# Performance work log

Hardware: AMD Instinct MI355X
Metric: run time of the kernel (lower is better)

The kernel has to match this reference:

```python
import jax, jax.numpy as jnp
import numpy as np
import math

B, L, D = 8, 2048, 768
ORDER, EMB = 128, 5
FFT = 2 * L
MIN_DECAY = math.log(0.01) / 1.5   # slow_decay_pct = 1.5
MAX_DECAY = math.log(0.01) / 0.3   # fast_decay_pct = 0.3
SHIFT = 0.0


def _pos_emb(seq_len, emb_dim):
    # pos_emb_init from the source: [t, Re(z), Im(z)] with bands = (emb_dim-1)//2
    bands = (emb_dim - 1) // 2
    t = jnp.linspace(0.0, 1.0, seq_len)[None, :, None]
    t_res = jnp.linspace(0.0, seq_len - 1, seq_len)[None, :, None]
    w = 2.0 * jnp.pi * t_res / seq_len
    f = jnp.linspace(1e-4, bands - 1, bands)[None, None]
    zc = jnp.exp(-1j * f * w)
    return jnp.concatenate([t, zc.real, zc.imag], axis=-1).astype(jnp.float32)  # (1, L, EMB)


def setup_inputs() -> dict:
    key = jax.random.key(0)
    ks = jax.random.split(key, 16)
    s = 0.02
    return {
        "u": jax.random.normal(ks[0], (B, L, D), jnp.float32),
        "in_W": jax.random.normal(ks[1], (D, 3 * D), jnp.float32) * s,
        "in_b": jnp.zeros((3 * D,), jnp.float32),
        "out_W": jax.random.normal(ks[2], (D, D), jnp.float32) * s,
        "out_b": jnp.zeros((D,), jnp.float32),
        "x1_s": jax.random.normal(ks[3], (D, 4), jnp.float32) * 0.25,
        "x2_s": jax.random.normal(ks[4], (D, 4), jnp.float32) * 0.25,
        "v_s": jax.random.normal(ks[5], (D, 4), jnp.float32) * 0.25,
        "x1_sb": jax.random.normal(ks[6], (D,), jnp.float32) * 0.1,
        "x2_sb": jax.random.normal(ks[7], (D,), jnp.float32) * 0.1,
        "v_sb": jax.random.normal(ks[8], (D,), jnp.float32) * 0.1,
        "D_bias": jax.random.normal(ks[9], (D,), jnp.float32),
        "z": _pos_emb(L, EMB),
        "sin_freq": 10.0 * jnp.ones((1, ORDER), jnp.float32),   # hyena_w = 10
        "eo_mat": jax.random.normal(ks[10], (1, EMB, ORDER), jnp.float32) * 0.3,
        "eo_bias": jnp.zeros((1, ORDER), jnp.float32),
        "oo1_mat": jax.random.normal(ks[11], (1, ORDER, ORDER), jnp.float32) * 0.08,
        "oo1_bias": jnp.zeros((1, ORDER), jnp.float32),
        "oo2_mat": jax.random.normal(ks[12], (1, ORDER, ORDER), jnp.float32) * 0.08,
        "oo2_bias": jnp.zeros((1, ORDER), jnp.float32),
        "oh_mat": jax.random.normal(ks[13], (1, ORDER, D), jnp.float32) * 0.08,
    }


def _depthwise4(x, w, b):
    # torch Conv1d(groups=3D, kernel=4, padding=3) truncated to [:L] == causal conv, left pad 3
    out = jax.lax.conv_general_dilated(
        x, w[:, None, :], window_strides=(1,), padding=[(3, 0)],
        dimension_numbers=("NCH", "OIH", "NCH"), feature_group_count=x.shape[1])
    return out + b[None, :, None]


def _hyena_filter(z, sin_freq, eo_mat, eo_bias, oo1_mat, oo1_bias, oo2_mat, oo2_bias, oh_mat):
    # then exponential decay modulation (exp_mod_in_place_fwd), channels=1, reverse=0.
    f = sin_freq[:, None, :]                                       # (1, 1, ORDER)
    h = jnp.sin(f * (jnp.einsum("cle,ceo->clo", z, eo_mat) + eo_bias[:, None, :]))
    h = jnp.sin(f * (jnp.einsum("clo,cop->clp", h, oo1_mat) + oo1_bias[:, None, :]))
    h = jnp.sin(f * (jnp.einsum("clo,cop->clp", h, oo2_mat) + oo2_bias[:, None, :]))
    k = jnp.einsum("clo,coh->clh", h, oh_mat)                      # (1, L, D)
    t = jnp.linspace(0.0, 1.0, k.shape[1])
    deltas = jnp.abs(jnp.linspace(MIN_DECAY, MAX_DECAY, k.shape[2]))
    k = k * (jnp.exp(-t[None, :, None] * deltas[None, None, :]) + SHIFT)
    return k[0].T                                                  # (D, L)


def _forward(u, in_W, in_b, out_W, out_b, x1_s, x2_s, v_s, x1_sb, x2_sb, v_sb,
             D_bias, z, sin_freq, eo_mat, eo_bias, oo1_mat, oo1_bias,
             oo2_mat, oo2_bias, oh_mat):
    seqlen = u.shape[1]
    k = _hyena_filter(z, sin_freq, eo_mat, eo_bias, oo1_mat, oo1_bias, oo2_mat, oo2_bias, oh_mat)
    x1x2v = u @ in_W + in_b                                        # (B, L, 3D)
    x1, x2, v = jnp.split(x1x2v, 3, axis=-1)
    x1 = jnp.transpose(x1, (0, 2, 1))                              # (B, D, L)
    x2 = jnp.transpose(x2, (0, 2, 1))
    v = jnp.transpose(v, (0, 2, 1))
    x1 = _depthwise4(x1, x1_s, x1_sb)
    x2 = _depthwise4(x2, x2_s, x2_sb)
    v = _depthwise4(v, v_s, v_sb)
    v = v * x1                                                     # first gate
    k_f = jnp.fft.rfft(k.astype(jnp.float32), n=FFT)               # (D, FFT//2+1)
    v_f = jnp.fft.rfft(v.astype(jnp.float32), n=FFT)               # (B, D, FFT//2+1)
    y = jnp.fft.irfft(v_f * k_f[None], n=FFT)[..., :seqlen]        # long FFT conv
    y = y + v * D_bias[None, :, None]                              # skip term
    y = y * x2                                                     # second gate
    y = jnp.transpose(y, (0, 2, 1))                                # (B, L, D)
    return y @ out_W + out_b


def reference(u, in_W, in_b, out_W, out_b, x1_s, x2_s, v_s, x1_sb, x2_sb, v_sb,
              D_bias, z, sin_freq, eo_mat, eo_bias, oo1_mat, oo1_bias,
              oo2_mat, oo2_bias, oh_mat):
    return _forward(u, in_W, in_b, out_W, out_b, x1_s, x2_s, v_s, x1_sb, x2_sb, v_sb,
                    D_bias, z, sin_freq, eo_mat, eo_bias, oo1_mat, oo1_bias,
                    oo2_mat, oo2_bias, oh_mat)
```

## Files before the change

kernel.cpp:

```cpp
#include <hip/hip_runtime.h>


typedef __bf16 bf16x8 __attribute__((ext_vector_type(8)));
typedef float  f32x4  __attribute__((ext_vector_type(4)));

#define AS1 __attribute__((address_space(1)))
#define AS3 __attribute__((address_space(3)))
#define GLD16(gp, lp) __builtin_amdgcn_global_load_lds((AS1 void*)(void*)(gp), (AS3 void*)(void*)(lp), 16, 0, 0)

#define LGKM_BAR       __asm__ __volatile__("s_waitcnt lgkmcnt(0)\n\ts_barrier" ::: "memory")
#define VM_LGKM_BAR(N) __asm__ __volatile__("s_waitcnt vmcnt(" #N ") lgkmcnt(0)\n\ts_barrier" ::: "memory")

__device__ __forceinline__ unsigned short f2b(float f) {
    unsigned u = __builtin_bit_cast(unsigned, f);
    unsigned r = (u + 0x7fffu + ((u >> 16) & 1u)) >> 16;
    return (unsigned short)r;
}
__device__ __forceinline__ float b2f(unsigned short h) {
    unsigned u = ((unsigned)h) << 16;
    return __builtin_bit_cast(float, u);
}
__device__ __forceinline__ float b2f_lo(unsigned u) {
    return __builtin_bit_cast(float, u << 16);
}
__device__ __forceinline__ float b2f_hi(unsigned u) {
    return __builtin_bit_cast(float, u & 0xffff0000u);
}

__device__ __forceinline__ float2 cmul(float2 a, float2 b) {
    return make_float2(a.x * b.x - a.y * b.y, a.x * b.y + a.y * b.x);
}
__device__ __forceinline__ float2 cadd(float2 a, float2 b) { return make_float2(a.x + b.x, a.y + b.y); }
__device__ __forceinline__ float2 csub(float2 a, float2 b) { return make_float2(a.x - b.x, a.y - b.y); }

#define BFLY(i,j)   { float2 ta=x[i], tb=x[j]; x[i]=cadd(ta,tb); x[j]=csub(ta,tb); }
#define BFLYW(i,j,w){ float2 ta=x[i], tb=x[j]; x[i]=cadd(ta,tb); x[j]=cmul(csub(ta,tb),(w)); }
#define BFLYI(i,j)  { float2 ta=x[i], tb=x[j]; x[i]=cadd(ta,tb); float2 tt=csub(ta,tb); x[j]=make_float2(-dd*tt.y, dd*tt.x); }
#define CSWAP(i,j)  { float2 tt=x[i]; x[i]=x[j]; x[j]=tt; }

template<int DIR, bool UZ>
__device__ __forceinline__ void dft16(float2* x) {
    const float dd = (float)DIR;
    const float C1 = 0.92387953251128674f, S1 = 0.38268343236508977f, R2 = 0.70710678118654752f;
    const float2 W1 = make_float2( C1, dd*S1);
    const float2 W2 = make_float2( R2, dd*R2);
    const float2 W3 = make_float2( S1, dd*C1);
    const float2 W5 = make_float2(-S1, dd*C1);
    const float2 W6 = make_float2(-R2, dd*R2);
    const float2 W7 = make_float2(-C1, dd*S1);
    if (UZ) {
        x[8]  = x[0];
        x[9]  = cmul(x[1], W1);
        x[10] = cmul(x[2], W2);
        x[11] = cmul(x[3], W3);
        x[12] = make_float2(-dd*x[4].y, dd*x[4].x);
        x[13] = cmul(x[5], W5);
        x[14] = cmul(x[6], W6);
        x[15] = cmul(x[7], W7);
    } else {
        BFLY(0,8); BFLYW(1,9,W1); BFLYW(2,10,W2); BFLYW(3,11,W3);
        BFLYI(4,12); BFLYW(5,13,W5); BFLYW(6,14,W6); BFLYW(7,15,W7);
    }
    BFLY(0,4);  BFLYW(1,5,W2);  BFLYI(2,6);   BFLYW(3,7,W6);
    BFLY(8,12); BFLYW(9,13,W2); BFLYI(10,14); BFLYW(11,15,W6);
    BFLY(0,2);  BFLYI(1,3);  BFLY(4,6);   BFLYI(5,7);
    BFLY(8,10); BFLYI(9,11); BFLY(12,14); BFLYI(13,15);
    BFLY(0,1); BFLY(2,3); BFLY(4,5); BFLY(6,7);
    BFLY(8,9); BFLY(10,11); BFLY(12,13); BFLY(14,15);
    CSWAP(1,8); CSWAP(2,4); CSWAP(3,12); CSWAP(5,10); CSWAP(7,14); CSWAP(11,13);
}

__device__ __forceinline__ void twiddle_mul(float2* x, float ang) {
    float s, c; __sincosf(ang, &s, &c);
    float2 w[16];
    w[1] = make_float2(c, s);
    w[2] = cmul(w[1], w[1]);
    w[3] = cmul(w[2], w[1]);  w[4] = cmul(w[2], w[2]);
    w[5] = cmul(w[4], w[1]);  w[6] = cmul(w[4], w[2]);
    w[7] = cmul(w[4], w[3]);  w[8] = cmul(w[4], w[4]);
    w[9]  = cmul(w[8], w[1]); w[10] = cmul(w[8], w[2]);
    w[11] = cmul(w[8], w[3]); w[12] = cmul(w[8], w[4]);
    w[13] = cmul(w[8], w[5]); w[14] = cmul(w[8], w[6]);
    w[15] = cmul(w[8], w[7]);
    #pragma unroll
    for (int k = 1; k < 16; ++k) x[k] = cmul(x[k], w[k]);
}

#define TWO_PI 6.283185307179586f
__device__ __forceinline__ void fft4096_fwd(float2* x, float2* lds, int t) {
    dft16<-1, true>(x);
    twiddle_mul(x, -(float)t * (TWO_PI / 4096.0f));
    #pragma unroll
    for (int k1 = 0; k1 < 16; ++k1) lds[k1 * 272 + t] = x[k1];
    __syncthreads();
    const int hi = t >> 4, lo = t & 15;
    #pragma unroll
    for (int t1 = 0; t1 < 16; ++t1) x[t1] = lds[hi * 272 + t1 * 16 + lo];
    dft16<-1, false>(x);
    twiddle_mul(x, -(float)lo * (TWO_PI / 256.0f));
    __syncthreads();
    #pragma unroll
    for (int k2 = 0; k2 < 16; ++k2) lds[t * 17 + k2] = x[k2];
    __syncthreads();
    #pragma unroll
    for (int t0 = 0; t0 < 16; ++t0) x[t0] = lds[(hi * 16 + t0) * 17 + lo];
    dft16<-1, false>(x);
}

__device__ __forceinline__ void fft4096_inv(float2* x, float2* lds, int t) {
    const int hi = t >> 4, lo = t & 15;
    dft16<1, false>(x);
    __syncthreads();
    #pragma unroll
    for (int t0 = 0; t0 < 16; ++t0) lds[(hi * 16 + t0) * 17 + lo] = x[t0];
    __syncthreads();
    #pragma unroll
    for (int k2 = 0; k2 < 16; ++k2) x[k2] = lds[t * 17 + k2];
    twiddle_mul(x, (float)lo * (TWO_PI / 256.0f));
    dft16<1, false>(x);
    __syncthreads();
    #pragma unroll
    for (int t1 = 0; t1 < 16; ++t1) lds[hi * 272 + t1 * 16 + lo] = x[t1];
    __syncthreads();
    #pragma unroll
    for (int k1 = 0; k1 < 16; ++k1) x[k1] = lds[k1 * 272 + t];
    twiddle_mul(x, (float)t * (TWO_PI / 4096.0f));
    dft16<1, false>(x);
}

__global__ __launch_bounds__(256) void filter_k_kernel(
    const float* __restrict__ z, const float* __restrict__ sf,
    const float* __restrict__ eo, const float* __restrict__ eo_b,
    const float* __restrict__ oo1, const float* __restrict__ oo1_b,
    const float* __restrict__ oo2, const float* __restrict__ oo2_b,
    const float* __restrict__ oh, float* __restrict__ kfil)
{
    __shared__ float h3buf[8][128];
    __shared__ float htmp[2][128];
    const int t = threadIdx.x;
    const int l0 = blockIdx.x * 8;
    const int half = t >> 7;
    const int o = t & 127;
    const float sfo = sf[o];
    for (int p = 0; p < 4; ++p) {
        const int li = p * 2 + half;
        const int l = l0 + li;
        float a = eo_b[o];
        #pragma unroll
        for (int e = 0; e < 5; ++e) a += z[l * 5 + e] * eo[e * 128 + o];
        htmp[half][o] = sinf(sfo * a);
        __syncthreads();
        float a2 = oo1_b[o];
        for (int q = 0; q < 128; ++q) a2 += htmp[half][q] * oo1[q * 128 + o];
        const float h2 = sinf(sfo * a2);
        __syncthreads();
        htmp[half][o] = h2;
        __syncthreads();
        float a3 = oo2_b[o];
        for (int q = 0; q < 128; ++q) a3 += htmp[half][q] * oo2[q * 128 + o];
        h3buf[li][o] = sinf(sfo * a3);
        __syncthreads();
    }
    const float MIND = -3.070113457325394f;
    const float MAXD = -15.350567286626972f;
    for (int c = 0; c < 3; ++c) {
        const int h = t + c * 256;
        float acc[8];
        #pragma unroll
        for (int li = 0; li < 8; ++li) acc[li] = 0.f;
        for (int q = 0; q < 128; ++q) {
            const float w = oh[q * 768 + h];
            #pragma unroll
            for (int li = 0; li < 8; ++li) acc[li] += h3buf[li][q] * w;
        }
        const float delta = fabsf(MIND + (MAXD - MIND) * (float)h * (1.0f / 767.0f));
        #pragma unroll
        for (int li = 0; li < 8; ++li) {
            const int l = l0 + li;
            const float tt = (float)l * (1.0f / 2047.0f);
            kfil[h * 2048 + l] = acc[li] * expf(-tt * delta);
        }
    }
}

__global__ __launch_bounds__(256, 4) void filter_fft_kernel(
    const float* __restrict__ kfil, float2* __restrict__ Kf)
{
    __shared__ float2 lds[4352];
    const int d = blockIdx.x, t = threadIdx.x;
    float2 x[16];
    #pragma unroll
    for (int r = 0; r < 8; ++r) x[r] = make_float2(kfil[d * 2048 + r * 256 + t], 0.f);
    fft4096_fwd(x, lds, t);
    #pragma unroll
    for (int k3 = 0; k3 < 16; ++k3) Kf[d * 4096 + k3 * 256 + t] = x[k3];
}

__global__ __launch_bounds__(256) void convert_u_kernel(
    const float* __restrict__ u, unsigned short* __restrict__ ub)
{
    const int g = blockIdx.x * 256 + threadIdx.x;
    const float4 v = ((const float4*)u)[g];
    uint2 o;
    o.x = (unsigned)f2b(v.x) | ((unsigned)f2b(v.y) << 16);
    o.y = (unsigned)f2b(v.z) | ((unsigned)f2b(v.w) << 16);
    ((uint2*)ub)[g] = o;
}

__global__ __launch_bounds__(256) void transpose_W_kernel(
    const float* __restrict__ W, unsigned short* __restrict__ Wt, int K, int N)
{
    __shared__ float tile[32][33];
    const int n0 = blockIdx.x * 32, k0 = blockIdx.y * 32;
    const int tx = threadIdx.x & 31, ty = threadIdx.x >> 5;
    #pragma unroll
    for (int r = 0; r < 4; ++r) {
        const int kk = ty + r * 8;
        tile[kk][tx] = W[(k0 + kk) * N + n0 + tx];
    }
    __syncthreads();
    #pragma unroll
    for (int r = 0; r < 4; ++r) {
        const int nn = ty + r * 8;
        Wt[(n0 + nn) * K + k0 + tx] = f2b(tile[tx][nn]);
    }
}

__global__ __launch_bounds__(256) void transpose_Y_kernel(
    const unsigned short* __restrict__ Y, unsigned short* __restrict__ Yt)
{
    __shared__ unsigned short tile[32][34];
    const int bx = blockIdx.x;
    const int l0 = (bx & 63) * 32;
    const int tmp = bx >> 6;
    const int d0 = (tmp % 24) * 32;
    const int b  = tmp / 24;
    const int tx = threadIdx.x & 31, ty = threadIdx.x >> 5;
    #pragma unroll
    for (int r = 0; r < 4; ++r) {
        const int dd = ty + r * 8;
        tile[dd][tx] = Y[(b * 768 + d0 + dd) * 2048 + l0 + tx];
    }
    __syncthreads();
    #pragma unroll
    for (int r = 0; r < 4; ++r) {
        const int ll = ty + r * 8;
        Yt[(b * 2048 + l0 + ll) * 768 + d0 + tx] = tile[tx][ll];
    }
}

__global__ __launch_bounds__(512, 2) void gemm256_kernel(
    const unsigned short* __restrict__ A,
    const unsigned short* __restrict__ Bm,
    const float* __restrict__ bias,
    unsigned short* __restrict__ outb,
    float* __restrict__ outf,
    int mode)
{
    extern __shared__ __align__(16) unsigned short lds[];
    unsigned short* As = lds;
    unsigned short* Bs = lds + 32768;
    const int t = threadIdx.x;
    const int wv = t >> 6, lane = t & 63;
    const int row0 = (mode == 0 ? blockIdx.y : blockIdx.x) * 256;
    const int col0 = (mode == 0 ? blockIdx.x : blockIdx.y) * 256;
    const int wr = wv >> 2, wc = wv & 3;
    const int frow = lane & 15, kc = lane >> 4;

    f32x4 acc[8][4] = {};

    const int srow = t >> 3;
    const int cdat = (t & 7) ^ (srow & 7);
    const unsigned short* gA = A  + (row0 + srow) * 768 + cdat * 8;
    const unsigned short* gB = Bm + (col0 + srow) * 768 + cdat * 8;

#define STG_A(buf, q, koff) GLD16(gA + (q) * 49152 + (koff), (char*)As + (buf) * 32768 + (q) * 8192 + wv * 1024)
#define STG_B(buf, q, koff) GLD16(gB + (q) * 49152 + (koff), (char*)Bs + (buf) * 32768 + (q) * 8192 + wv * 1024)

    const int sx = frow & 7;
    const int aRowBase = (wr * 128 + frow) * 64;
    const int bRowBase = (wc * 64 + frow) * 64;
    const int sl0 = ((0 + kc) ^ sx) * 8;
    const int sl1 = ((4 + kc) ^ sx) * 8;

    bf16x8 aF[4][2], bN0[2][2], bN1[2][2];

#define READ_A(buf, mh)                                                         \
    _Pragma("unroll") for (int m = 0; m < 4; ++m) {                             \
        aF[m][0] = *(const bf16x8*)(As + (buf) * 16384 + aRowBase + ((mh) * 4 + m) * 1024 + sl0); \
        aF[m][1] = *(const bf16x8*)(As + (buf) * 16384 + aRowBase + ((mh) * 4 + m) * 1024 + sl1); \
    }
#define READ_B(buf, nh, arr)                                                    \
    _Pragma("unroll") for (int n = 0; n < 2; ++n) {                             \
        arr[n][0] = *(const bf16x8*)(Bs + (buf) * 16384 + bRowBase + ((nh) * 2 + n) * 1024 + sl0); \
        arr[n][1] = *(const bf16x8*)(Bs + (buf) * 16384 + bRowBase + ((nh) * 2 + n) * 1024 + sl1); \
    }
#define MFMA_Q(mh, nh, arr)                                                     \
    __builtin_amdgcn_s_setprio(1);                                              \
    _Pragma("unroll") for (int m = 0; m < 4; ++m)                               \
    _Pragma("unroll") for (int n = 0; n < 2; ++n)                               \
    _Pragma("unroll") for (int ks = 0; ks < 2; ++ks)                            \
        acc[(mh) * 4 + m][(nh) * 2 + n] = __builtin_amdgcn_mfma_f32_16x16x32_bf16( \
            aF[m][ks], arr[n][ks], acc[(mh) * 4 + m][(nh) * 2 + n], 0, 0, 0);   \
    __builtin_amdgcn_s_setprio(0);

    STG_A(0, 0, 0); STG_A(0, 1, 0); STG_A(0, 2, 0); STG_A(0, 3, 0);
    STG_B(0, 0, 0); STG_B(0, 1, 0); STG_B(0, 2, 0); STG_B(0, 3, 0);
    STG_A(1, 0, 64); STG_A(1, 2, 64);
    STG_B(1, 0, 64); STG_B(1, 1, 64); STG_B(1, 2, 64); STG_B(1, 3, 64);
    VM_LGKM_BAR(6);

    for (int i = 0; i < 5; ++i) {
        const int k1 = (2 * i + 1) * 64, k2 = (2 * i + 2) * 64, k3 = (2 * i + 3) * 64;
        READ_A(0, 0); READ_B(0, 0, bN0);
        STG_A(1, 1, k1); STG_A(1, 3, k1);
        MFMA_Q(0, 0, bN0);
        LGKM_BAR;
        READ_B(0, 1, bN1);
        STG_A(0, 0, k2); STG_A(0, 2, k2);
        MFMA_Q(0, 1, bN1);
        LGKM_BAR;
        READ_A(0, 1);
        STG_B(0, 0, k2); STG_B(0, 1, k2);
        MFMA_Q(1, 1, bN1);
        LGKM_BAR;
        STG_B(0, 2, k2); STG_B(0, 3, k2);
        MFMA_Q(1, 0, bN0);
        VM_LGKM_BAR(6);
        READ_A(1, 0); READ_B(1, 0, bN0);
        STG_A(0, 1, k2); STG_A(0, 3, k2);
        MFMA_Q(0, 0, bN0);
        LGKM_BAR;
        READ_B(1, 1, bN1);
        STG_A(1, 0, k3); STG_A(1, 2, k3);
        MFMA_Q(0, 1, bN1);
        LGKM_BAR;
        READ_A(1, 1);
        STG_B(1, 0, k3); STG_B(1, 1, k3);
        MFMA_Q(1, 1, bN1);
        LGKM_BAR;
        STG_B(1, 2, k3); STG_B(1, 3, k3);
        MFMA_Q(1, 0, bN0);
        VM_LGKM_BAR(6);
    }

    {
        READ_A(0, 0); READ_B(0, 0, bN0);
        STG_A(1, 1, 704); STG_A(1, 3, 704);
        MFMA_Q(0, 0, bN0);
        LGKM_BAR;
        READ_B(0, 1, bN1);
        MFMA_Q(0, 1, bN1);
        LGKM_BAR;
        READ_A(0, 1);
        MFMA_Q(1, 1, bN1);
        LGKM_BAR;
        MFMA_Q(1, 0, bN0);
        VM_LGKM_BAR(2);
        READ_A(1, 0); READ_B(1, 0, bN0);
        MFMA_Q(0, 0, bN0);
        LGKM_BAR;
        READ_B(1, 1, bN1);
        MFMA_Q(0, 1, bN1);
        VM_LGKM_BAR(0);
        READ_A(1, 1);
        MFMA_Q(1, 1, bN1);
        MFMA_Q(1, 0, bN0);
    }
#undef READ_A
#undef READ_B
#undef MFMA_Q
#undef STG_A
#undef STG_B

    if (mode == 0) {
        const int part = row0 / 768;
        const int bb = col0 / 2048;
        unsigned short* Xp = outb + (size_t)(part * 8 + bb) * 768 * 2048;
        const int drow0 = row0 - part * 768 + wr * 128 + (lane >> 4) * 4;
        const int lcol0 = col0 - bb * 2048 + wc * 64 + frow;
        #pragma unroll
        for (int m = 0; m < 8; ++m) {
            #pragma unroll
            for (int rr = 0; rr < 4; ++rr) {
                const int dd = drow0 + m * 16 + rr;
                const float bn = bias[row0 + wr * 128 + (lane >> 4) * 4 + m * 16 + rr];
                #pragma unroll
                for (int n = 0; n < 4; ++n)
                    Xp[dd * 2048 + lcol0 + n * 16] = f2b(acc[m][n][rr] + bn);
            }
        }
    } else {
        #pragma unroll
        for (int m = 0; m < 8; ++m) {
            #pragma unroll
            for (int rr = 0; rr < 4; ++rr) {
                const int mm = row0 + wr * 128 + (lane >> 4) * 4 + m * 16 + rr;
                #pragma unroll
                for (int n = 0; n < 4; ++n) {
                    const int nn = col0 + wc * 64 + n * 16 + frow;
                    outf[(size_t)mm * 768 + nn] = acc[m][n][rr] + bias[nn];
                }
            }
        }
    }
}

__device__ __forceinline__ void conv6(const unsigned short* __restrict__ p,
                                      const float* w, float bias, int t, float* out8)
{
    const uint4 m = *(const uint4*)(p + 8 * t);
    uint2 q = make_uint2(0u, 0u);
    if (t) q = *(const uint2*)(p + 8 * t - 4);
    float s[12];
    s[0] = b2f_lo(q.x); s[1] = b2f_hi(q.x); s[2] = b2f_lo(q.y); s[3] = b2f_hi(q.y);
    s[4] = b2f_lo(m.x); s[5] = b2f_hi(m.x); s[6] = b2f_lo(m.y); s[7] = b2f_hi(m.y);
    s[8] = b2f_lo(m.z); s[9] = b2f_hi(m.z); s[10] = b2f_lo(m.w); s[11] = b2f_hi(m.w);
    #pragma unroll
    for (int i = 0; i < 8; ++i)
        out8[i] = bias + w[0] * s[i + 1] + w[1] * s[i + 2] + w[2] * s[i + 3] + w[3] * s[i + 4];
}

__global__ __launch_bounds__(256, 4) void fft_conv_kernel(
    const unsigned short* __restrict__ X, const float2* __restrict__ Kf,
    const float* __restrict__ x1_s, const float* __restrict__ x2_s, const float* __restrict__ v_s,
    const float* __restrict__ x1_sb, const float* __restrict__ x2_sb, const float* __restrict__ v_sb,
    const float* __restrict__ D_bias, unsigned short* __restrict__ Y)
{
    __shared__ __align__(16) float2 lds[4352];
    unsigned* ldsu = (unsigned*)lds;
    const int d = blockIdx.x, jp = blockIdx.y, t = threadIdx.x;
    const int b0 = jp * 2, b1 = b0 + 1;

    float w1[4], w2[4], wv[4];
    #pragma unroll
    for (int j = 0; j < 4; ++j) { w1[j] = x1_s[d * 4 + j]; w2[j] = x2_s[d * 4 + j]; wv[j] = v_s[d * 4 + j]; }
    const float bc1 = x1_sb[d], bc2 = x2_sb[d], bcv = v_sb[d], Db = D_bias[d];

    const unsigned short* px1a = X + ((size_t)(0 * 8 + b0) * 768 + d) * 2048;
    const unsigned short* px2a = X + ((size_t)(1 * 8 + b0) * 768 + d) * 2048;
    const unsigned short* pva  = X + ((size_t)(2 * 8 + b0) * 768 + d) * 2048;
    const unsigned short* px1b = X + ((size_t)(0 * 8 + b1) * 768 + d) * 2048;
    const unsigned short* px2b = X + ((size_t)(1 * 8 + b1) * 768 + d) * 2048;
    const unsigned short* pvb  = X + ((size_t)(2 * 8 + b1) * 768 + d) * 2048;

    {
        float x1a[8], x2a[8], vva[8];
        conv6(px1a, w1, bc1, t, x1a);
        conv6(px2a, w2, bc2, t, x2a);
        conv6(pva,  wv, bcv, t, vva);
        float x1b[8], x2b[8], vvb[8];
        conv6(px1b, w1, bc1, t, x1b);
        conv6(px2b, w2, bc2, t, x2b);
        conv6(pvb,  wv, bcv, t, vvb);
        unsigned vh_pk[8], c2_pk[8];
        #pragma unroll
        for (int i = 0; i < 8; ++i) {
            vh_pk[i] = (unsigned)f2b(vva[i] * x1a[i]) | ((unsigned)f2b(vvb[i] * x1b[i]) << 16);
            c2_pk[i] = (unsigned)f2b(x2a[i]) | ((unsigned)f2b(x2b[i]) << 16);
        }
        *(uint4*)(ldsu + 8 * t)        = make_uint4(vh_pk[0], vh_pk[1], vh_pk[2], vh_pk[3]);
        *(uint4*)(ldsu + 8 * t + 4)    = make_uint4(vh_pk[4], vh_pk[5], vh_pk[6], vh_pk[7]);
        *(uint4*)(ldsu + 2048 + 8 * t)     = make_uint4(c2_pk[0], c2_pk[1], c2_pk[2], c2_pk[3]);
        *(uint4*)(ldsu + 2048 + 8 * t + 4) = make_uint4(c2_pk[4], c2_pk[5], c2_pk[6], c2_pk[7]);
    }
    __syncthreads();

    unsigned vhp[8], c2p[8];
    float2 x[16];
    #pragma unroll
    for (int r = 0; r < 8; ++r) {
        const unsigned u = ldsu[r * 256 + t];
        vhp[r] = u;
        x[r] = make_float2(b2f_lo(u), b2f_hi(u));
    }
    #pragma unroll
    for (int r = 0; r < 8; ++r) c2p[r] = ldsu[2048 + r * 256 + t];

    const float2* kf = Kf + (size_t)d * 4096;
    float2 kfr[16];
    #pragma unroll
    for (int k3 = 0; k3 < 16; ++k3) kfr[k3] = kf[k3 * 256 + t];

    __syncthreads();

    fft4096_fwd(x, lds, t);
    #pragma unroll
    for (int k3 = 0; k3 < 16; ++k3) x[k3] = cmul(x[k3], kfr[k3]);
    fft4096_inv(x, lds, t);

    const float invN = 1.0f / 4096.0f;
    unsigned short* ya = Y + ((size_t)b0 * 768 + d) * 2048;
    unsigned short* yb = Y + ((size_t)b1 * 768 + d) * 2048;
    #pragma unroll
    for (int n1 = 0; n1 < 8; ++n1) {
        const int l = n1 * 256 + t;
        const float va = b2f_lo(vhp[n1]);
        const float vb = b2f_hi(vhp[n1]);
        const float ca = b2f_lo(c2p[n1]);
        const float cb = b2f_hi(c2p[n1]);
        ya[l] = f2b((x[n1].x * invN + va * Db) * ca);
        yb[l] = f2b((x[n1].y * invN + vb * Db) * cb);
    }
}

extern "C" void kernel_launch(void* const* d_in, const int* in_sizes, int n_in,
                              void* d_out, int out_size, void* d_ws, size_t ws_size,
                              hipStream_t stream)
{
    (void)in_sizes; (void)n_in; (void)out_size; (void)ws_size;
    const float* u      = (const float*)d_in[0];
    const float* in_W   = (const float*)d_in[1];
    const float* in_b   = (const float*)d_in[2];
    const float* out_W  = (const float*)d_in[3];
    const float* out_b  = (const float*)d_in[4];
    const float* x1_s   = (const float*)d_in[5];
    const float* x2_s   = (const float*)d_in[6];
    const float* v_s    = (const float*)d_in[7];
    const float* x1_sb  = (const float*)d_in[8];
    const float* x2_sb  = (const float*)d_in[9];
    const float* v_sb   = (const float*)d_in[10];
    const float* D_bias = (const float*)d_in[11];
    const float* z      = (const float*)d_in[12];
    const float* sf     = (const float*)d_in[13];
    const float* eo     = (const float*)d_in[14];
    const float* eo_b   = (const float*)d_in[15];
    const float* oo1    = (const float*)d_in[16];
    const float* oo1_b  = (const float*)d_in[17];
    const float* oo2    = (const float*)d_in[18];
    const float* oo2_b  = (const float*)d_in[19];
    const float* oh     = (const float*)d_in[20];
    float* out = (float*)d_out;

    char* ws = (char*)d_ws;
    unsigned short* Xbf  = (unsigned short*)(ws + 0);
    unsigned short* Ybf  = (unsigned short*)(ws + 75497472);
    unsigned short* ubYt = (unsigned short*)(ws + 100663296);
    unsigned short* Wt   = (unsigned short*)(ws + 125829120);
    unsigned short* W2t  = (unsigned short*)(ws + 129368064);
    float*          kfil = (float*)(ws + 130547712);
    float2*         Kf   = (float2*)(ws + 136839168);

    static int attr_set = 0;
    if (!attr_set) {
        (void)hipFuncSetAttribute(reinterpret_cast<const void*>(gemm256_kernel),
                                  hipFuncAttributeMaxDynamicSharedMemorySize, 131072);
        attr_set = 1;
    }

    filter_k_kernel<<<256, 256, 0, stream>>>(z, sf, eo, eo_b, oo1, oo1_b, oo2, oo2_b, oh, kfil);
    filter_fft_kernel<<<768, 256, 0, stream>>>(kfil, Kf);
    convert_u_kernel<<<12288, 256, 0, stream>>>(u, ubYt);
    transpose_W_kernel<<<dim3(72, 24), 256, 0, stream>>>(in_W, Wt, 768, 2304);
    transpose_W_kernel<<<dim3(24, 24), 256, 0, stream>>>(out_W, W2t, 768, 768);
    gemm256_kernel<<<dim3(64, 9), 512, 131072, stream>>>(Wt, ubYt, in_b, Xbf, nullptr, 0);
    fft_conv_kernel<<<dim3(768, 4), 256, 0, stream>>>(Xbf, Kf, x1_s, x2_s, v_s, x1_sb, x2_sb, v_sb, D_bias, Ybf);
    transpose_Y_kernel<<<12288, 256, 0, stream>>>(Ybf, ubYt);
    gemm256_kernel<<<dim3(64, 3), 512, 131072, stream>>>(ubYt, W2t, out_b, nullptr, out, 1);
}
```

Measured before the change: 395.7 us.

## Use precomputed twiddle tables and XOR-swizzled LDS in FFT, raise occupancy

```diff
diff --git a/kernel.cpp b/kernel.cpp
--- a/kernel.cpp
+++ b/kernel.cpp
@@ -30,8 +30,31 @@
 __device__ __forceinline__ float2 cmul(float2 a, float2 b) {
     return make_float2(a.x * b.x - a.y * b.y, a.x * b.y + a.y * b.x);
 }
+__device__ __forceinline__ float2 cmulc(float2 a, float2 b) {
+    return make_float2(a.x * b.x + a.y * b.y, a.y * b.x - a.x * b.y);
+}
 __device__ __forceinline__ float2 cadd(float2 a, float2 b) { return make_float2(a.x + b.x, a.y + b.y); }
 __device__ __forceinline__ float2 csub(float2 a, float2 b) { return make_float2(a.x - b.x, a.y - b.y); }
+
+#define TWO_PI 6.283185307179586f
+__device__ float2 d_Tw1[4096];
+__device__ float2 d_Tw2[256];
+
+__global__ __launch_bounds__(256) void twiddle_init_kernel() {
+    const int i = blockIdx.x * 256 + threadIdx.x;
+    if (i < 4096) {
+        const int tt = i >> 4, k = i & 15;
+        float s, c;
+        __sincosf(-(float)(tt * k) * (TWO_PI / 4096.0f), &s, &c);
+        d_Tw1[i] = make_float2(c, s);
+    } else {
+        const int j = i - 4096;
+        const int lo = j >> 4, k = j & 15;
+        float s, c;
+        __sincosf(-(float)(lo * k) * (TWO_PI / 256.0f), &s, &c);
+        d_Tw2[j] = make_float2(c, s);
+    }
+}
 
 #define BFLY(i,j)   { float2 ta=x[i], tb=x[j]; x[i]=cadd(ta,tb); x[j]=csub(ta,tb); }
 #define BFLYW(i,j,w){ float2 ta=x[i], tb=x[j]; x[i]=cadd(ta,tb); x[j]=cmul(csub(ta,tb),(w)); }
@@ -70,61 +93,61 @@
     CSWAP(1,8); CSWAP(2,4); CSWAP(3,12); CSWAP(5,10); CSWAP(7,14); CSWAP(11,13);
 }
 
-__device__ __forceinline__ void twiddle_mul(float2* x, float ang) {
-    float s, c; __sincosf(ang, &s, &c);
+__device__ __forceinline__ int ph1(int row, int col) { return row * 256 + (col ^ row); }
+__device__ __forceinline__ int ph2(int row, int col) { return row * 16 + (col ^ (row & 15)); }
+
+__device__ __forceinline__ void fft4096_fwd(float2* x, float2* lds, int t) {
     float2 w[16];
-    w[1] = make_float2(c, s);
-    w[2] = cmul(w[1], w[1]);
-    w[3] = cmul(w[2], w[1]);  w[4] = cmul(w[2], w[2]);
-    w[5] = cmul(w[4], w[1]);  w[6] = cmul(w[4], w[2]);
-    w[7] = cmul(w[4], w[3]);  w[8] = cmul(w[4], w[4]);
-    w[9]  = cmul(w[8], w[1]); w[10] = cmul(w[8], w[2]);
-    w[11] = cmul(w[8], w[3]); w[12] = cmul(w[8], w[4]);
-    w[13] = cmul(w[8], w[5]); w[14] = cmul(w[8], w[6]);
-    w[15] = cmul(w[8], w[7]);
+    #pragma unroll
+    for (int k = 1; k < 16; ++k) w[k] = d_Tw1[t * 16 + k];
+    dft16<-1, true>(x);
     #pragma unroll
     for (int k = 1; k < 16; ++k) x[k] = cmul(x[k], w[k]);
-}
-
-#define TWO_PI 6.283185307179586f
-__device__ __forceinline__ void fft4096_fwd(float2* x, float2* lds, int t) {
-    dft16<-1, true>(x);
-    twiddle_mul(x, -(float)t * (TWO_PI / 4096.0f));
-    #pragma unroll
-    for (int k1 = 0; k1 < 16; ++k1) lds[k1 * 272 + t] = x[k1];
+    #pragma unroll
+    for (int k1 = 0; k1 < 16; ++k1) lds[ph1(k1, t)] = x[k1];
     __syncthreads();
     const int hi = t >> 4, lo = t & 15;
     #pragma unroll
-    for (int t1 = 0; t1 < 16; ++t1) x[t1] = lds[hi * 272 + t1 * 16 + lo];
+    for (int t1 = 0; t1 < 16; ++t1) x[t1] = lds[ph1(hi, t1 * 16 + lo)];
+    #pragma unroll
+    for (int k = 1; k < 16; ++k) w[k] = d_Tw2[lo * 16 + k];
     dft16<-1, false>(x);
-    twiddle_mul(x, -(float)lo * (TWO_PI / 256.0f));
-    __syncthreads();
-    #pragma unroll
-    for (int k2 = 0; k2 < 16; ++k2) lds[t * 17 + k2] = x[k2];
-    __syncthreads();
-    #pragma unroll
-    for (int t0 = 0; t0 < 16; ++t0) x[t0] = lds[(hi * 16 + t0) * 17 + lo];
+    #pragma unroll
+    for (int k = 1; k < 16; ++k) x[k] = cmul(x[k], w[k]);
+    __syncthreads();
+    #pragma unroll
+    for (int k2 = 0; k2 < 16; ++k2) lds[ph2(t, k2)] = x[k2];
+    __syncthreads();
+    #pragma unroll
+    for (int t0 = 0; t0 < 16; ++t0) x[t0] = lds[ph2(hi * 16 + t0, lo)];
     dft16<-1, false>(x);
 }
 
 __device__ __forceinline__ void fft4096_inv(float2* x, float2* lds, int t) {
     const int hi = t >> 4, lo = t & 15;
+    float2 w[16];
     dft16<1, false>(x);
     __syncthreads();
     #pragma unroll
-    for (int t0 = 0; t0 < 16; ++t0) lds[(hi * 16 + t0) * 17 + lo] = x[t0];
-    __syncthreads();
-    #pragma unroll
-    for (int k2 = 0; k2 < 16; ++k2) x[k2] = lds[t * 17 + k2];
-    twiddle_mul(x, (float)lo * (TWO_PI / 256.0f));
+    for (int t0 = 0; t0 < 16; ++t0) lds[ph2(hi * 16 + t0, lo)] = x[t0];
+    #pragma unroll
+    for (int k = 1; k < 16; ++k) w[k] = d_Tw2[lo * 16 + k];
+    __syncthreads();
+    #pragma unroll
+    for (int k2 = 0; k2 < 16; ++k2) x[k2] = lds[ph2(t, k2)];
+    #pragma unroll
+    for (int k = 1; k < 16; ++k) x[k] = cmulc(x[k], w[k]);
     dft16<1, false>(x);
     __syncthreads();
     #pragma unroll
-    for (int t1 = 0; t1 < 16; ++t1) lds[hi * 272 + t1 * 16 + lo] = x[t1];
-    __syncthreads();
-    #pragma unroll
-    for (int k1 = 0; k1 < 16; ++k1) x[k1] = lds[k1 * 272 + t];
-    twiddle_mul(x, (float)t * (TWO_PI / 4096.0f));
+    for (int t1 = 0; t1 < 16; ++t1) lds[ph1(hi, t1 * 16 + lo)] = x[t1];
+    #pragma unroll
+    for (int k = 1; k < 16; ++k) w[k] = d_Tw1[t * 16 + k];
+    __syncthreads();
+    #pragma unroll
+    for (int k1 = 0; k1 < 16; ++k1) x[k1] = lds[ph1(k1, t)];
+    #pragma unroll
+    for (int k = 1; k < 16; ++k) x[k] = cmulc(x[k], w[k]);
     dft16<1, false>(x);
 }
 
@@ -135,14 +158,14 @@
     const float* __restrict__ oo2, const float* __restrict__ oo2_b,
     const float* __restrict__ oh, float* __restrict__ kfil)
 {
-    __shared__ float h3buf[8][128];
+    __shared__ float h3buf[4][128];
     __shared__ float htmp[2][128];
     const int t = threadIdx.x;
-    const int l0 = blockIdx.x * 8;
+    const int l0 = blockIdx.x * 4;
     const int half = t >> 7;
     const int o = t & 127;
     const float sfo = sf[o];
-    for (int p = 0; p < 4; ++p) {
+    for (int p = 0; p < 2; ++p) {
         const int li = p * 2 + half;
         const int l = l0 + li;
         float a = eo_b[o];
@@ -165,17 +188,17 @@
     const float MAXD = -15.350567286626972f;
     for (int c = 0; c < 3; ++c) {
         const int h = t + c * 256;
-        float acc[8];
+        float acc[4];
         #pragma unroll
-        for (int li = 0; li < 8; ++li) acc[li] = 0.f;
+        for (int li = 0; li < 4; ++li) acc[li] = 0.f;
         for (int q = 0; q < 128; ++q) {
             const float w = oh[q * 768 + h];
             #pragma unroll
-            for (int li = 0; li < 8; ++li) acc[li] += h3buf[li][q] * w;
+            for (int li = 0; li < 4; ++li) acc[li] += h3buf[li][q] * w;
         }
         const float delta = fabsf(MIND + (MAXD - MIND) * (float)h * (1.0f / 767.0f));
         #pragma unroll
-        for (int li = 0; li < 8; ++li) {
+        for (int li = 0; li < 4; ++li) {
             const int l = l0 + li;
             const float tt = (float)l * (1.0f / 2047.0f);
             kfil[h * 2048 + l] = acc[li] * expf(-tt * delta);
@@ -183,17 +206,19 @@
     }
 }
 
-__global__ __launch_bounds__(256, 4) void filter_fft_kernel(
+__global__ __launch_bounds__(256, 5) void filter_fft_kernel(
     const float* __restrict__ kfil, float2* __restrict__ Kf)
 {
-    __shared__ float2 lds[4352];
+    __shared__ __align__(16) float2 lds[4096];
     const int d = blockIdx.x, t = threadIdx.x;
     float2 x[16];
     #pragma unroll
     for (int r = 0; r < 8; ++r) x[r] = make_float2(kfil[d * 2048 + r * 256 + t], 0.f);
     fft4096_fwd(x, lds, t);
-    #pragma unroll
-    for (int k3 = 0; k3 < 16; ++k3) Kf[d * 4096 + k3 * 256 + t] = x[k3];
+    const float s = 1.0f / 4096.0f;
+    #pragma unroll
+    for (int k3 = 0; k3 < 16; ++k3)
+        Kf[d * 4096 + k3 * 256 + t] = make_float2(x[k3].x * s, x[k3].y * s);
 }
 
 __global__ __launch_bounds__(256) void convert_u_kernel(
@@ -421,13 +446,13 @@
         out8[i] = bias + w[0] * s[i + 1] + w[1] * s[i + 2] + w[2] * s[i + 3] + w[3] * s[i + 4];
 }
 
-__global__ __launch_bounds__(256, 4) void fft_conv_kernel(
+__global__ __launch_bounds__(256, 5) void fft_conv_kernel(
     const unsigned short* __restrict__ X, const float2* __restrict__ Kf,
     const float* __restrict__ x1_s, const float* __restrict__ x2_s, const float* __restrict__ v_s,
     const float* __restrict__ x1_sb, const float* __restrict__ x2_sb, const float* __restrict__ v_sb,
     const float* __restrict__ D_bias, unsigned short* __restrict__ Y)
 {
-    __shared__ __align__(16) float2 lds[4352];
+    __shared__ __align__(16) float2 lds[4096];
     unsigned* ldsu = (unsigned*)lds;
     const int d = blockIdx.x, jp = blockIdx.y, t = threadIdx.x;
     const int b0 = jp * 2, b1 = b0 + 1;
@@ -489,7 +514,6 @@
     for (int k3 = 0; k3 < 16; ++k3) x[k3] = cmul(x[k3], kfr[k3]);
     fft4096_inv(x, lds, t);
 
-    const float invN = 1.0f / 4096.0f;
     unsigned short* ya = Y + ((size_t)b0 * 768 + d) * 2048;
     unsigned short* yb = Y + ((size_t)b1 * 768 + d) * 2048;
     #pragma unroll
@@ -499,8 +523,8 @@
         const float vb = b2f_hi(vhp[n1]);
         const float ca = b2f_lo(c2p[n1]);
         const float cb = b2f_hi(c2p[n1]);
-        ya[l] = f2b((x[n1].x * invN + va * Db) * ca);
-        yb[l] = f2b((x[n1].y * invN + vb * Db) * cb);
+        ya[l] = f2b((x[n1].x + va * Db) * ca);
+        yb[l] = f2b((x[n1].y + vb * Db) * cb);
     }
 }
 
@@ -548,7 +572,8 @@
         attr_set = 1;
     }
 
-    filter_k_kernel<<<256, 256, 0, stream>>>(z, sf, eo, eo_b, oo1, oo1_b, oo2, oo2_b, oh, kfil);
+    twiddle_init_kernel<<<17, 256, 0, stream>>>();
+    filter_k_kernel<<<512, 256, 0, stream>>>(z, sf, eo, eo_b, oo1, oo1_b, oo2, oo2_b, oh, kfil);
     filter_fft_kernel<<<768, 256, 0, stream>>>(kfil, Kf);
     convert_u_kernel<<<12288, 256, 0, stream>>>(u, ubYt);
     transpose_W_kernel<<<dim3(72, 24), 256, 0, stream>>>(in_W, Wt, 768, 2304);
```

New measurement: 496.9 us. +25.6%, slower.
